# Performance work log

Hardware: AMD Instinct MI355X
Metric: run time of the kernel (lower is better)

## Reference

```python
import jax, jax.numpy as jnp
import numpy as np

N_RAYS = 16384
PTS_PER_RAY = 256
M = N_RAYS * PTS_PER_RAY
ALPHA_INIT = 0.01


def setup_inputs() -> dict:
    key = jax.random.key(0)
    k1, k2 = jax.random.split(key)
    density = jax.random.normal(k1, (M,), dtype=jnp.float32)
    ray_id = jnp.sort(jax.random.randint(k2, (M,), 0, N_RAYS)).astype(jnp.int32)
    shift = jnp.full((1,), np.log(1.0 / (1.0 - ALPHA_INIT) - 1.0), dtype=jnp.float32)
    interval = jnp.full((1,), 0.5, dtype=jnp.float32)
    return {"density": density, "ray_id": ray_id, "shift": shift, "interval": interval, "N": N_RAYS}


def reference(density, ray_id, shift, interval, N):
    # Raw2Alpha: alpha = 1 - exp(-softplus(density + shift) * interval)
    #           => log(1 - alpha) = -softplus(density + shift) * interval (exact, stable)
    sp = jax.nn.softplus(density + shift[0])            # [M]
    log_one_minus_alpha = -sp * interval[0]             # [M], <= 0
    alpha = -jnp.expm1(log_one_minus_alpha)             # [M]

    # Alphas2Weights: per-ray exclusive cumprod of (1-alpha) in log space.
    cs = jnp.cumsum(log_one_minus_alpha)                # inclusive global cumsum
    ex = cs - log_one_minus_alpha                       # exclusive global cumsum (non-increasing)
    # value of ex at the first element of each ray = segment max (ex is non-increasing)
    base = jax.ops.segment_max(ex, ray_id, num_segments=N)  # [N]
    T = jnp.exp(ex - base[ray_id])                      # exclusive per-ray transmittance
    weights = T * alpha                                 # [M]
    # alphainv_last = prod(1-alpha) over each ray (empty rays -> 1)
    log_total = jax.ops.segment_sum(log_one_minus_alpha, ray_id, num_segments=N)
    alphainv_last = jnp.exp(log_total)                  # [N]
    return weights, alphainv_last
```

## Files before the change

kernel.cpp:

```cpp
#include <hip/hip_runtime.h>
#include <hip/hip_bf16.h>


#define ELEMS_PER_LANE 6
#define CHUNK (64 * ELEMS_PER_LANE)

__device__ __forceinline__ float wave_incl_scan(float x) {
    float v = x;
    v += __int_as_float(__builtin_amdgcn_update_dpp(0, __float_as_int(v), 0x111, 0xf, 0xf, true));
    v += __int_as_float(__builtin_amdgcn_update_dpp(0, __float_as_int(v), 0x112, 0xf, 0xf, true));
    v += __int_as_float(__builtin_amdgcn_update_dpp(0, __float_as_int(v), 0x114, 0xf, 0xf, true));
    v += __int_as_float(__builtin_amdgcn_update_dpp(0, __float_as_int(v), 0x118, 0xf, 0xf, true));
    v += __int_as_float(__builtin_amdgcn_update_dpp(0, __float_as_int(v), 0x142, 0xa, 0xf, false));
    v += __int_as_float(__builtin_amdgcn_update_dpp(0, __float_as_int(v), 0x143, 0xc, 0xf, false));
    return v;
}

__global__ void VoxelNeRF_find_starts(const int* __restrict__ ray_id,
                                      int* __restrict__ start,
                                      int M, int N) {
    const int j  = blockIdx.x * blockDim.x + threadIdx.x;
    const int i0 = j * 4;
    if (i0 >= M) return;
    const int4 v = *reinterpret_cast<const int4*>(ray_id + i0);
    int prev = (i0 == 0) ? -1 : ray_id[i0 - 1];
    const int ids0 = v.x, ids1 = v.y, ids2 = v.z, ids3 = v.w;
    #pragma unroll
    for (int k = 0; k < 4; ++k) {
        const int cur = (k == 0) ? ids0 : (k == 1) ? ids1 : (k == 2) ? ids2 : ids3;
        if (cur != prev) {
            for (int r = prev + 1; r <= cur; ++r) start[r] = i0 + k;
        }
        prev = cur;
    }
    if (i0 + 4 >= M) {
        for (int r = prev + 1; r <= N; ++r) start[r] = M;
    }
}

__global__ __launch_bounds__(256) void VoxelNeRF_scan(
    const float* __restrict__ density,
    const int*   __restrict__ start,
    const float* __restrict__ shift_p,
    const float* __restrict__ interval_p,
    float* __restrict__ weights,
    float* __restrict__ alphainv_last,
    int N) {
    const int wave = threadIdx.x >> 6;
    const int lane = threadIdx.x & 63;
    const int r = blockIdx.x * 4 + wave;
    if (r >= N) return;

    const int s = start[r];
    const int e = start[r + 1];
    const float shift    = shift_p[0];
    const float interval = interval_p[0];

    float carry = 0.0f;

    for (int base = s; base < e; base += CHUNK) {
        const int i0 = base + lane * ELEMS_PER_LANE;

        float lm[ELEMS_PER_LANE];
        float al[ELEMS_PER_LANE];
        float pk[ELEMS_PER_LANE];
        float lane_sum = 0.0f;

        #pragma unroll
        for (int k = 0; k < ELEMS_PER_LANE; ++k) {
            const int i = i0 + k;
            float lomk = 0.0f, alk = 0.0f;
            if (i < e) {
                const float x  = density[i] + shift;
                const float sp = fmaxf(x, 0.0f) + __logf(1.0f + __expf(-fabsf(x)));
                lomk = -sp * interval;
                alk  = 1.0f - __expf(lomk);
            }
            lm[k] = lomk;
            al[k] = alk;
            pk[k] = lane_sum;
            lane_sum += lomk;
        }

        const float v_incl = wave_incl_scan(lane_sum);
        const float excl_lane = carry + (v_incl - lane_sum);

        #pragma unroll
        for (int k = 0; k < ELEMS_PER_LANE; ++k) {
            const int i = i0 + k;
            if (i < e) {
                weights[i] = __expf(excl_lane + pk[k]) * al[k];
            }
        }

        carry += __int_as_float(__builtin_amdgcn_readlane(__float_as_int(v_incl), 63));
    }

    if (lane == 0) {
        alphainv_last[r] = __expf(carry);
    }
}

extern "C" void kernel_launch(void* const* d_in, const int* in_sizes, int n_in,
                              void* d_out, int out_size, void* d_ws, size_t ws_size,
                              hipStream_t stream) {
    const float* density    = (const float*)d_in[0];
    const int*   ray_id     = (const int*)d_in[1];
    const float* shift_p    = (const float*)d_in[2];
    const float* interval_p = (const float*)d_in[3];
    const int M = in_sizes[0];
    const int N = out_size - M;

    float* weights       = (float*)d_out;
    float* alphainv_last = (float*)d_out + M;
    int*   start         = (int*)d_ws;

    {
        const int threads = 256;
        const int elems   = (M + 3) / 4;
        const int blocks  = (elems + threads - 1) / threads;
        VoxelNeRF_find_starts<<<blocks, threads, 0, stream>>>(ray_id, start, M, N);
    }
    {
        const int waves_per_block = 4;
        const int blocks = (N + waves_per_block - 1) / waves_per_block;
        VoxelNeRF_scan<<<blocks, 256, 0, stream>>>(
            density, start, shift_p, interval_p, weights, alphainv_last, N);
    }
}
```

Measured before the change: 95.54 us.

## Fuse ray-start search into scan kernel via galloping binary search, vectorize I/O

Removes the separate find_starts pass that read all of ray_id and wrote a start array. Each wave now locates its ray's segment bounds with a galloping lower-bound search seeded from the expected position r*M/N. Chunks are aligned to 8 elements so density loads and weight stores can use float4 where the chunk is fully inside the ray. This saves a full pass over ray_id (16 MB) and a kernel launch, at the cost of dependent scattered loads during the search and some wasted lanes at segment edges.

```diff
diff --git a/kernel.cpp b/kernel.cpp
--- a/kernel.cpp
+++ b/kernel.cpp
@@ -2,8 +2,8 @@
 #include <hip/hip_bf16.h>
 
 
-#define ELEMS_PER_LANE 6
-#define CHUNK (64 * ELEMS_PER_LANE)
+#define EPL 8
+#define CHUNK (64 * EPL)
 
 __device__ __forceinline__ float wave_incl_scan(float x) {
     float v = x;
@@ -16,80 +16,112 @@
     return v;
 }
 
-__global__ void VoxelNeRF_find_starts(const int* __restrict__ ray_id,
-                                      int* __restrict__ start,
-                                      int M, int N) {
-    const int j  = blockIdx.x * blockDim.x + threadIdx.x;
-    const int i0 = j * 4;
-    if (i0 >= M) return;
-    const int4 v = *reinterpret_cast<const int4*>(ray_id + i0);
-    int prev = (i0 == 0) ? -1 : ray_id[i0 - 1];
-    const int ids0 = v.x, ids1 = v.y, ids2 = v.z, ids3 = v.w;
-    #pragma unroll
-    for (int k = 0; k < 4; ++k) {
-        const int cur = (k == 0) ? ids0 : (k == 1) ? ids1 : (k == 2) ? ids2 : ids3;
-        if (cur != prev) {
-            for (int r = prev + 1; r <= cur; ++r) start[r] = i0 + k;
-        }
-        prev = cur;
+__device__ __forceinline__ int lower_bound_gallop(const int* __restrict__ a,
+                                                  int M, int key, int hint) {
+    if (hint < 0) hint = 0;
+    if (hint >= M) hint = M - 1;
+    int lo, hi;
+    if (a[hint] >= key) {
+        int step = 32;
+        hi = hint;
+        lo = hint - step;
+        while (lo >= 0 && a[lo] >= key) { hi = lo; step <<= 1; lo = hint - step; }
+        if (lo < 0) lo = -1;
+    } else {
+        int step = 32;
+        lo = hint;
+        hi = hint + step;
+        while (hi < M && a[hi] < key) { lo = hi; step <<= 1; hi = hint + step; }
+        if (hi > M) hi = M;
     }
-    if (i0 + 4 >= M) {
-        for (int r = prev + 1; r <= N; ++r) start[r] = M;
+    while (hi - lo > 1) {
+        const int mid = (lo + hi) >> 1;
+        if (a[mid] >= key) hi = mid; else lo = mid;
     }
+    return hi;
 }
 
-__global__ __launch_bounds__(256) void VoxelNeRF_scan(
+__global__ __launch_bounds__(256) void VoxelNeRF_fused(
     const float* __restrict__ density,
-    const int*   __restrict__ start,
+    const int*   __restrict__ ray_id,
     const float* __restrict__ shift_p,
     const float* __restrict__ interval_p,
     float* __restrict__ weights,
     float* __restrict__ alphainv_last,
-    int N) {
+    int M, int N) {
     const int wave = threadIdx.x >> 6;
     const int lane = threadIdx.x & 63;
     const int r = blockIdx.x * 4 + wave;
     if (r >= N) return;
 
-    const int s = start[r];
-    const int e = start[r + 1];
+    const int avg  = M / N;
+    const int s = lower_bound_gallop(ray_id, M, r,     (int)(((long long)r * M) / N));
+    const int e = lower_bound_gallop(ray_id, M, r + 1, s + avg);
+
     const float shift    = shift_p[0];
     const float interval = interval_p[0];
 
     float carry = 0.0f;
+    const int a0 = s & ~(EPL - 1);
 
-    for (int base = s; base < e; base += CHUNK) {
-        const int i0 = base + lane * ELEMS_PER_LANE;
+    for (int base = a0; base < e; base += CHUNK) {
+        const int g = base + lane * EPL;
 
-        float lm[ELEMS_PER_LANE];
-        float al[ELEMS_PER_LANE];
-        float pk[ELEMS_PER_LANE];
+        float x8[EPL];
+        if (g < e && g + EPL <= M) {
+            const float4* p = reinterpret_cast<const float4*>(density + g);
+            const float4 v0 = p[0];
+            const float4 v1 = p[1];
+            x8[0] = v0.x; x8[1] = v0.y; x8[2] = v0.z; x8[3] = v0.w;
+            x8[4] = v1.x; x8[5] = v1.y; x8[6] = v1.z; x8[7] = v1.w;
+        } else if (g < e) {
+            #pragma unroll
+            for (int k = 0; k < EPL; ++k) {
+                const int i = g + k;
+                x8[k] = (i < M) ? density[i] : 0.0f;
+            }
+        }
+
+        float al[EPL], pk[EPL];
         float lane_sum = 0.0f;
-
         #pragma unroll
-        for (int k = 0; k < ELEMS_PER_LANE; ++k) {
-            const int i = i0 + k;
+        for (int k = 0; k < EPL; ++k) {
+            const int i = g + k;
             float lomk = 0.0f, alk = 0.0f;
-            if (i < e) {
-                const float x  = density[i] + shift;
+            if (i >= s && i < e) {
+                const float x  = x8[k] + shift;
                 const float sp = fmaxf(x, 0.0f) + __logf(1.0f + __expf(-fabsf(x)));
                 lomk = -sp * interval;
                 alk  = 1.0f - __expf(lomk);
             }
-            lm[k] = lomk;
             al[k] = alk;
             pk[k] = lane_sum;
             lane_sum += lomk;
         }
 
-        const float v_incl = wave_incl_scan(lane_sum);
-        const float excl_lane = carry + (v_incl - lane_sum);
+        const float v_incl  = wave_incl_scan(lane_sum);
+        const float base_ex = carry + (v_incl - lane_sum);
 
-        #pragma unroll
-        for (int k = 0; k < ELEMS_PER_LANE; ++k) {
-            const int i = i0 + k;
-            if (i < e) {
-                weights[i] = __expf(excl_lane + pk[k]) * al[k];
+        if (g >= s && g + EPL <= e) {
+            float4 w0, w1;
+            w0.x = __expf(base_ex + pk[0]) * al[0];
+            w0.y = __expf(base_ex + pk[1]) * al[1];
+            w0.z = __expf(base_ex + pk[2]) * al[2];
+            w0.w = __expf(base_ex + pk[3]) * al[3];
+            w1.x = __expf(base_ex + pk[4]) * al[4];
+            w1.y = __expf(base_ex + pk[5]) * al[5];
+            w1.z = __expf(base_ex + pk[6]) * al[6];
+            w1.w = __expf(base_ex + pk[7]) * al[7];
+            float4* q = reinterpret_cast<float4*>(weights + g);
+            q[0] = w0;
+            q[1] = w1;
+        } else if (g + EPL > s && g < e) {
+            #pragma unroll
+            for (int k = 0; k < EPL; ++k) {
+                const int i = g + k;
+                if (i >= s && i < e) {
+                    weights[i] = __expf(base_ex + pk[k]) * al[k];
+                }
             }
         }
 
@@ -113,18 +145,9 @@
 
     float* weights       = (float*)d_out;
     float* alphainv_last = (float*)d_out + M;
-    int*   start         = (int*)d_ws;
 
-    {
-        const int threads = 256;
-        const int elems   = (M + 3) / 4;
-        const int blocks  = (elems + threads - 1) / threads;
-        VoxelNeRF_find_starts<<<blocks, threads, 0, stream>>>(ray_id, start, M, N);
-    }
-    {
-        const int waves_per_block = 4;
-        const int blocks = (N + waves_per_block - 1) / waves_per_block;
-        VoxelNeRF_scan<<<blocks, 256, 0, stream>>>(
-            density, start, shift_p, interval_p, weights, alphainv_last, N);
-    }
+    const int waves_per_block = 4;
+    const int blocks = (N + waves_per_block - 1) / waves_per_block;
+    VoxelNeRF_fused<<<blocks, 256, 0, stream>>>(
+        density, ray_id, shift_p, interval_p, weights, alphainv_last, M, N);
 }
```

New measurement: 99.97 us. +4.6%, slower.
